# Kernel tuning notes

Hardware: AMD Instinct MI355X
Metric: run time of the kernel (lower is better)

The kernel has to match this reference:

```python
import jax, jax.numpy as jnp
import numpy as np
import math

def _ln(x, g, b, eps=1e-5):
    mu = x.mean(-1, keepdims=True)
    var = ((x - mu) ** 2).mean(-1, keepdims=True)
    return (x - mu) / jnp.sqrt(var + eps) * g + b

def _mha(x, in_w, in_b, out_w, out_b, nh):
    # torch nn.MultiheadAttention (batch_first, eval): q,k,v chunks of in_proj
    Bn, Nn, Dm = x.shape
    hd = Dm // nh
    q, k, v = jnp.split(x @ in_w.T + in_b, 3, axis=-1)
    sp = lambda t: t.reshape(Bn, Nn, nh, hd).transpose(0, 2, 1, 3)
    q, k, v = sp(q), sp(k), sp(v)
    a = jax.nn.softmax(jnp.einsum('bhid,bhjd->bhij', q, k) / math.sqrt(hd), axis=-1)
    y = jnp.einsum('bhij,bhjd->bhid', a, v).transpose(0, 2, 1, 3).reshape(Bn, Nn, Dm)
    return y @ out_w.T + out_b

def setup_inputs():
    key = jax.random.key(0)
    ks = iter(jax.random.split(key, 40))
    nrm = lambda shape: jax.random.normal(next(ks), shape, jnp.float32) * 0.02
    B, T, C, H, W = 2, 32, 3, 64, 64
    D, P, nL, nS = 512, 8, 6, 3
    N = (H // P) ** 2
    z = lambda *s: jnp.zeros(s, jnp.float32)
    o = lambda *s: jnp.ones(s, jnp.float32)
    return dict(
        x=jax.random.normal(next(ks), (B, T, C, H, W), jnp.float32),
        patch_w=nrm((D, C * P * P)), patch_b=z(D),
        tok_ln_g=o(D), tok_ln_b=z(D),
        spatial_pos=nrm((1, 1, N, D)), temporal_pos=nrm((1, T, 1, D)),
        snorm_g=o(D), snorm_b=z(D),
        sa_in_w=nrm((nS, 3 * D, D)), sa_in_b=z(nS, 3 * D),
        sa_out_w=nrm((nS, D, D)), sa_out_b=z(nS, D),
        ln1_g=o(nL, D), ln1_b=z(nL, D),
        kqv_w=nrm((nL, 3 * D, D)), kqv_b=z(nL, 3 * D),
        proj_w=nrm((nL, D, D)), proj_b=z(nL, D),
        ln2_g=o(nL, D), ln2_b=z(nL, D),
        fc_w=nrm((nL, 4 * D, D)), fc_b=z(nL, 4 * D),
        cproj_w=nrm((nL, D, 4 * D)), cproj_b=z(nL, D),
        lnf_g=o(D), lnf_b=z(D),
        th_w1=nrm((D // 2, D)), th_b1=z(D // 2), th_w2=nrm((1, D // 2)), th_b2=z(1),
        sh_w1=nrm((D // 2, D)), sh_b1=z(D // 2), sh_w2=nrm((1, D // 2)), sh_b2=z(1),
        pf_w1=nrm((D // 2, D)), pf_b1=z(D // 2), pf_w2=nrm((1, D // 2)), pf_b2=z(1),
    )

def reference(x, patch_w, patch_b, tok_ln_g, tok_ln_b, spatial_pos, temporal_pos,
              snorm_g, snorm_b, sa_in_w, sa_in_b, sa_out_w, sa_out_b,
              ln1_g, ln1_b, kqv_w, kqv_b, proj_w, proj_b, ln2_g, ln2_b,
              fc_w, fc_b, cproj_w, cproj_b, lnf_g, lnf_b,
              th_w1, th_b1, th_w2, th_b2, sh_w1, sh_b1, sh_w2, sh_b2,
              pf_w1, pf_b1, pf_w2, pf_b2):
    B, T, C, H, W = x.shape
    D = patch_w.shape[0]
    P = int(math.isqrt(patch_w.shape[1] // C))
    Hn, Wn = H // P, W // P
    N = Hn * Wn
    # Conv3d kernel=(1,P,P), stride=(1,P,P) == per-frame patchify + matmul
    patches = x.reshape(B, T, C, Hn, P, Wn, P).transpose(0, 1, 3, 5, 2, 4, 6).reshape(B, T, N, C * P * P)
    tok = _ln(patches @ patch_w.T + patch_b, tok_ln_g, tok_ln_b)
    tok = tok + spatial_pos + temporal_pos[:, :T]
    # per-frame spatial attention: identical math per frame -> batch over B*T
    s = tok.reshape(B * T, N, D)
    for i in range(sa_in_w.shape[0]):
        s = s + _mha(_ln(s, snorm_g, snorm_b), sa_in_w[i], sa_in_b[i], sa_out_w[i], sa_out_b[i], nh=4)
    L = T * N
    hid = s.reshape(B, L, D)
    nh = 8
    hd = D // nh
    mask = jnp.tril(jnp.ones((L, L), bool))  # causal over T*N tokens
    for i in range(kqv_w.shape[0]):
        a_in = _ln(hid, ln1_g[i], ln1_b[i])
        k, q, v = jnp.split(a_in @ kqv_w[i].T + kqv_b[i], 3, axis=-1)  # torch split order: k, q, v
        sp = lambda t: t.reshape(B, L, nh, hd).transpose(0, 2, 1, 3)
        q, k, v = sp(q), sp(k), sp(v)
        att = jnp.einsum('bhid,bhjd->bhij', q, k) / math.sqrt(hd)
        att = jax.nn.softmax(jnp.where(mask, att, -jnp.inf), axis=-1)
        y = jnp.einsum('bhij,bhjd->bhid', att, v).transpose(0, 2, 1, 3).reshape(B, L, D)
        hid = hid + y @ proj_w[i].T + proj_b[i]
        m_in = _ln(hid, ln2_g[i], ln2_b[i])
        h = jax.nn.gelu(m_in @ fc_w[i].T + fc_b[i], approximate=False)
        hid = hid + h @ cproj_w[i].T + cproj_b[i]
    hid = _ln(hid, lnf_g, lnf_b).reshape(B, T, N, D)
    head = lambda zz, w1, b1, w2, b2: jax.nn.leaky_relu(zz @ w1.T + b1, 0.2) @ w2.T + b2
    tf = hid.mean(axis=2)  # [B, T, D]
    temporal_score = head(tf[:, -1], th_w1, th_b1, th_w2, th_b2)  # [B, 1] (last timestep, full lengths)
    spatial_score = head(hid.mean(axis=1).mean(axis=1), sh_w1, sh_b1, sh_w2, sh_b2)
    per_frame_scores = head(tf, pf_w1, pf_b1, pf_w2, pf_b2)  # [B, T, 1]
    final_score = temporal_score + spatial_score + per_frame_scores.mean(axis=1)
    return (temporal_score, spatial_score, per_frame_scores, final_score)
```

## Files before the change

kernel.cpp:

```cpp
#include <hip/hip_runtime.h>
#include <hip/hip_bf16.h>
#include <math.h>

#define MTOK 4096

typedef __bf16 bf16x8 __attribute__((ext_vector_type(8)));
typedef float f32x4 __attribute__((ext_vector_type(4)));

__device__ __forceinline__ ushort f2bf(float f){
  __hip_bfloat16 h = __float2bfloat16(f);
  return *reinterpret_cast<ushort*>(&h);
}
__device__ __forceinline__ float bf2f(ushort u){
  return __uint_as_float(((uint)u) << 16);
}
__device__ __forceinline__ void gload_lds16(const void* g, void* l){
  __builtin_amdgcn_global_load_lds((__attribute__((address_space(1))) void*)(void*)g,
                                   (__attribute__((address_space(3))) void*)l, 16, 0, 0);
}

__device__ __forceinline__ float blockReduceSum(float v, float* red){
  #pragma unroll
  for (int off = 32; off; off >>= 1) v += __shfl_down(v, off, 64);
  int lane = threadIdx.x & 63, wid = threadIdx.x >> 6;
  __syncthreads();
  if (lane == 0) red[wid] = v;
  __syncthreads();
  float r = 0.f;
  int nw = blockDim.x >> 6;
  for (int i = 0; i < nw; i++) r += red[i];
  return r;
}
__device__ __forceinline__ float rowMax16(float v){
  #pragma unroll
  for (int m = 8; m; m >>= 1) v = fmaxf(v, __shfl_xor(v, m, 64));
  return v;
}
__device__ __forceinline__ float rowSum16(float v){
  #pragma unroll
  for (int m = 8; m; m >>= 1) v += __shfl_xor(v, m, 64);
  return v;
}

__global__ __launch_bounds__(256) void cvt_w_kernel(
    const float* __restrict__ src, ushort* __restrict__ dst, int n)
{
  int i = (blockIdx.x * 256 + threadIdx.x) * 8;
  float4 a = *(const float4*)(src + i);
  float4 b = *(const float4*)(src + i + 4);
  uint4 o;
  o.x = (uint)f2bf(a.x) | ((uint)f2bf(a.y) << 16);
  o.y = (uint)f2bf(a.z) | ((uint)f2bf(a.w) << 16);
  o.z = (uint)f2bf(b.x) | ((uint)f2bf(b.y) << 16);
  o.w = (uint)f2bf(b.z) | ((uint)f2bf(b.w) << 16);
  *(uint4*)(dst + i) = o;
}

#define OFF_PATCH 0u
#define OFF_SAIN  98304u
#define OFF_SAOUT 2457600u
#define OFF_KQV   3244032u
#define OFF_PROJ  7962624u
#define OFF_FC    9535488u
#define OFF_CPROJ 15826944u
#define W_TOTAL   22118400u
__global__ __launch_bounds__(256) void cvt_all_kernel(
    const float* __restrict__ pw, const float* __restrict__ sain,
    const float* __restrict__ saout, const float* __restrict__ kqv,
    const float* __restrict__ proj, const float* __restrict__ fc,
    const float* __restrict__ cproj, ushort* __restrict__ dst)
{
  int blk = blockIdx.x;
  const float* src; size_t off;
  if      (blk <    48){ src = pw;    off = OFF_PATCH; }
  else if (blk <  1200){ src = sain;  off = OFF_SAIN;  blk -= 48;   }
  else if (blk <  1584){ src = saout; off = OFF_SAOUT; blk -= 1200; }
  else if (blk <  3888){ src = kqv;   off = OFF_KQV;   blk -= 1584; }
  else if (blk <  4656){ src = proj;  off = OFF_PROJ;  blk -= 3888; }
  else if (blk <  7728){ src = fc;    off = OFF_FC;    blk -= 4656; }
  else                 { src = cproj; off = OFF_CPROJ; blk -= 7728; }
  size_t si = (size_t)blk*2048 + threadIdx.x*8;
  float4 a = *(const float4*)(src + si);
  float4 b = *(const float4*)(src + si + 4);
  uint4 o;
  o.x = (uint)f2bf(a.x) | ((uint)f2bf(a.y) << 16);
  o.y = (uint)f2bf(a.z) | ((uint)f2bf(a.w) << 16);
  o.z = (uint)f2bf(b.x) | ((uint)f2bf(b.y) << 16);
  o.w = (uint)f2bf(b.z) | ((uint)f2bf(b.w) << 16);
  *(uint4*)(dst + off + si) = o;
}

__global__ __launch_bounds__(256) void im2col_kernel(
    const float* __restrict__ x, ushort* __restrict__ Pm)
{
  int idx = blockIdx.x*256 + threadIdx.x;
  int m = idx / 24, e8 = idx % 24;
  int b = m >> 11, t = (m >> 6) & 31, n = m & 63;
  int hn = n >> 3, wn = n & 7;
  int c = e8 >> 3, ph = e8 & 7;
  const float* src = x + (((size_t)(b*32 + t)*3 + c)*64 + hn*8 + ph)*64 + wn*8;
  float4 a = *(const float4*)src;
  float4 bq = *(const float4*)(src + 4);
  uint4 o;
  o.x = (uint)f2bf(a.x) | ((uint)f2bf(a.y) << 16);
  o.y = (uint)f2bf(a.z) | ((uint)f2bf(a.w) << 16);
  o.z = (uint)f2bf(bq.x) | ((uint)f2bf(bq.y) << 16);
  o.w = (uint)f2bf(bq.z) | ((uint)f2bf(bq.w) << 16);
  *(uint4*)(Pm + (size_t)m*192 + e8*8) = o;
}

__global__ __launch_bounds__(256) void ln_pos_kernel(
    const float* __restrict__ in, float* __restrict__ out,
    const float* __restrict__ g, const float* __restrict__ b,
    const float* __restrict__ spos, const float* __restrict__ tpos)
{
  int r = blockIdx.x*4 + (threadIdx.x >> 6);
  int lane = threadIdx.x & 63;
  int n = r & 63, t = (r >> 6) & 31;
  const float* row = in + (size_t)r*512 + lane*8;
  float4 v0 = *(const float4*)row;
  float4 v1 = *(const float4*)(row + 4);
  float s = v0.x+v0.y+v0.z+v0.w+v1.x+v1.y+v1.z+v1.w;
  float q = v0.x*v0.x+v0.y*v0.y+v0.z*v0.z+v0.w*v0.w+v1.x*v1.x+v1.y*v1.y+v1.z*v1.z+v1.w*v1.w;
  #pragma unroll
  for (int m = 1; m < 64; m <<= 1){ s += __shfl_xor(s, m, 64); q += __shfl_xor(q, m, 64); }
  float mu = s*(1.f/512.f);
  float inv = rsqrtf(q*(1.f/512.f) - mu*mu + 1e-5f);
  const float* gp = g + lane*8;
  const float* bp = b + lane*8;
  const float* sp = spos + n*512 + lane*8;
  const float* tp = tpos + t*512 + lane*8;
  float* op = out + (size_t)r*512 + lane*8;
  #pragma unroll
  for (int e = 0; e < 2; e++){
    float4 vv = e ? v1 : v0;
    float4 gg = *(const float4*)(gp + e*4);
    float4 bb = *(const float4*)(bp + e*4);
    float4 ss = *(const float4*)(sp + e*4);
    float4 tt = *(const float4*)(tp + e*4);
    float4 oo;
    oo.x = (vv.x-mu)*inv*gg.x + bb.x + ss.x + tt.x;
    oo.y = (vv.y-mu)*inv*gg.y + bb.y + ss.y + tt.y;
    oo.z = (vv.z-mu)*inv*gg.z + bb.z + ss.z + tt.z;
    oo.w = (vv.w-mu)*inv*gg.w + bb.w + ss.w + tt.w;
    *(float4*)(op + e*4) = oo;
  }
}

__global__ __launch_bounds__(256) void ln_bf16_kernel(
    const float* __restrict__ in, ushort* __restrict__ out,
    const float* __restrict__ g, const float* __restrict__ b)
{
  int r = blockIdx.x*4 + (threadIdx.x >> 6);
  int lane = threadIdx.x & 63;
  const float* row = in + (size_t)r*512 + lane*8;
  float4 v0 = *(const float4*)row;
  float4 v1 = *(const float4*)(row + 4);
  float s = v0.x+v0.y+v0.z+v0.w+v1.x+v1.y+v1.z+v1.w;
  float q = v0.x*v0.x+v0.y*v0.y+v0.z*v0.z+v0.w*v0.w+v1.x*v1.x+v1.y*v1.y+v1.z*v1.z+v1.w*v1.w;
  #pragma unroll
  for (int m = 1; m < 64; m <<= 1){ s += __shfl_xor(s, m, 64); q += __shfl_xor(q, m, 64); }
  float mu = s*(1.f/512.f);
  float inv = rsqrtf(q*(1.f/512.f) - mu*mu + 1e-5f);
  float4 g0 = *(const float4*)(g + lane*8);
  float4 g1 = *(const float4*)(g + lane*8 + 4);
  float4 b0 = *(const float4*)(b + lane*8);
  float4 b1 = *(const float4*)(b + lane*8 + 4);
  uint4 o;
  o.x = (uint)f2bf((v0.x-mu)*inv*g0.x + b0.x) | ((uint)f2bf((v0.y-mu)*inv*g0.y + b0.y) << 16);
  o.y = (uint)f2bf((v0.z-mu)*inv*g0.z + b0.z) | ((uint)f2bf((v0.w-mu)*inv*g0.w + b0.w) << 16);
  o.z = (uint)f2bf((v1.x-mu)*inv*g1.x + b1.x) | ((uint)f2bf((v1.y-mu)*inv*g1.y + b1.y) << 16);
  o.w = (uint)f2bf((v1.z-mu)*inv*g1.z + b1.z) | ((uint)f2bf((v1.w-mu)*inv*g1.w + b1.w) << 16);
  *(uint4*)(out + (size_t)r*512 + lane*8) = o;
}

template<int BM, int BN, bool GELU, bool BF16OUT>
__global__ __launch_bounds__(256) void gemm2_kernel(
    const ushort* __restrict__ X, const ushort* __restrict__ Wb,
    const float* __restrict__ bias, const float* __restrict__ res,
    void* __restrict__ Yv, int M, int Nn, int K)
{
  constexpr int WROWS = (BN == 128) ? 2 : 4;
  constexpr int WM = BM / WROWS;
  constexpr int FM = WM / 16;
  constexpr int FN = 4;
  __shared__ __attribute__((aligned(16))) char smem[2*(BM+BN)*128];
  char* Xs0 = smem;
  char* Ws0 = smem + BM*128;
  char* Xs1 = smem + (BM+BN)*128;
  char* Ws1 = Xs1 + BM*128;
  int tid = threadIdx.x, lane = tid & 63, wv = tid >> 6;
  int bm = blockIdx.y * BM, bn = blockIdx.x * BN;
  int wm, wn;
  if (BN == 128){ wm = (wv >> 1) * WM; wn = (wv & 1) * 64; }
  else          { wm = wv * WM;        wn = 0; }

  f32x4 acc[FM][FN];
  #pragma unroll
  for (int i = 0; i < FM; i++)
    #pragma unroll
    for (int j = 0; j < FN; j++){ f32x4 z = {0.f,0.f,0.f,0.f}; acc[i][j] = z; }

  int rowoff = wv*8 + (lane >> 3);
  int colsrc = ((lane & 7) ^ (lane >> 3)) * 16;

  auto stage = [&](char* Xd, char* Wd, int k0){
    #pragma unroll
    for (int i = 0; i < BM/32; i++){
      int row = i*32 + rowoff;
      gload_lds16((const char*)(X + (size_t)(bm + row)*K + k0) + colsrc,
                  Xd + (i*32 + wv*8)*128);
    }
    #pragma unroll
    for (int i = 0; i < BN/32; i++){
      int row = i*32 + rowoff;
      gload_lds16((const char*)(Wb + (size_t)(bn + row)*K + k0) + colsrc,
                  Wd + (i*32 + wv*8)*128);
    }
  };

  stage(Xs0, Ws0, 0);
  __syncthreads();
  int nt = K >> 6;
  for (int t = 0; t < nt; t++){
    char* Xc = (t & 1) ? Xs1 : Xs0;
    char* Wc = (t & 1) ? Ws1 : Ws0;
    if (t + 1 < nt) stage((t & 1) ? Xs0 : Xs1, (t & 1) ? Ws0 : Ws1, (t+1)*64);
    #pragma unroll
    for (int kc = 0; kc < 2; kc++){
      bf16x8 a[FM], b[FN];
      #pragma unroll
      for (int f = 0; f < FM; f++){
        int ra = wm + f*16 + (lane & 15);
        a[f] = *(const bf16x8*)(Xc + ra*128 + ((kc*64 + (lane>>4)*16) ^ ((ra & 7) << 4)));
      }
      #pragma unroll
      for (int f = 0; f < FN; f++){
        int rb = wn + f*16 + (lane & 15);
        b[f] = *(const bf16x8*)(Wc + rb*128 + ((kc*64 + (lane>>4)*16) ^ ((rb & 7) << 4)));
      }
      #pragma unroll
      for (int i = 0; i < FM; i++)
        #pragma unroll
        for (int j = 0; j < FN; j++)
          acc[i][j] = __builtin_amdgcn_mfma_f32_16x16x32_bf16(a[i], b[j], acc[i][j], 0, 0, 0);
    }
    __syncthreads();
  }
  int col0 = lane & 15;
  float bv[FN];
  #pragma unroll
  for (int fn = 0; fn < FN; fn++) bv[fn] = bias[bn + wn + fn*16 + col0];
  #pragma unroll
  for (int fm = 0; fm < FM; fm++){
    #pragma unroll
    for (int r = 0; r < 4; r++){
      int m = bm + wm + fm*16 + (lane >> 4)*4 + r;
      #pragma unroll
      for (int fn = 0; fn < FN; fn++){
        int n = bn + wn + fn*16 + col0;
        float v = acc[fm][fn][r] + bv[fn];
        if (res) v += res[(size_t)m*Nn + n];
        if (GELU) v = 0.5f * v * (1.f + erff(v * 0.70710678118654752440f));
        if (BF16OUT) ((ushort*)Yv)[(size_t)m*Nn + n] = f2bf(v);
        else         ((float*) Yv)[(size_t)m*Nn + n] = v;
      }
    }
  }
}

__global__ __launch_bounds__(256) void spatial_attn_mfma_kernel(
    const ushort* __restrict__ qkv, ushort* __restrict__ y)
{
  __shared__ __attribute__((aligned(16))) char Ks[64*256];
  __shared__ __attribute__((aligned(16))) char Vt[128*128];
  __shared__ __attribute__((aligned(16))) char Ps[64*128];
  int bt = blockIdx.x, h = blockIdx.y;
  int tid = threadIdx.x, lane = tid & 63, w = tid >> 6;
  const ushort* base = qkv + (size_t)bt*64*1536 + (size_t)h*128;
  const float scale = 0.08838834764831845f;

  int qrow = w*16 + (lane & 15);
  bf16x8 qa[4];
  #pragma unroll
  for (int kc = 0; kc < 4; kc++)
    qa[kc] = *(const bf16x8*)(base + (size_t)qrow*1536 + kc*32 + (lane>>4)*8);

  #pragma unroll
  for (int i = 0; i < 4; i++){
    int row = w*16 + i*4 + (lane >> 4);
    const char* src = (const char*)(base + (size_t)row*1536 + 512) + (((lane & 15) ^ (row & 15)) * 16);
    char* dst = Ks + (w*16 + i*4)*256;
    gload_lds16(src, dst);
  }
  {
    int vj = (tid & 31) * 2;
    int d0 = (tid >> 5) * 16;
    const ushort* v0p = base + (size_t)vj*1536 + 1024 + d0;
    const ushort* v1p = v0p + 1536;
    uint4 a0 = *(const uint4*)(v0p);
    uint4 a1 = *(const uint4*)(v0p + 8);
    uint4 b0 = *(const uint4*)(v1p);
    uint4 b1 = *(const uint4*)(v1p + 8);
    uint av[8] = {a0.x, a0.y, a0.z, a0.w, a1.x, a1.y, a1.z, a1.w};
    uint bv[8] = {b0.x, b0.y, b0.z, b0.w, b1.x, b1.y, b1.z, b1.w};
    int cb = 4 * (tid & 31);
    #pragma unroll
    for (int e = 0; e < 8; e++){
      int dl = d0 + e*2, dh = dl + 1;
      uint vlo = (av[e] & 0xffffu) | ((bv[e] & 0xffffu) << 16);
      uint vhi = (av[e] >> 16) | (bv[e] & 0xffff0000u);
      *(uint*)(Vt + dl*128 + (cb ^ ((dl & 7) << 4))) = vlo;
      *(uint*)(Vt + dh*128 + (cb ^ ((dh & 7) << 4))) = vhi;
    }
  }
  __syncthreads();

  f32x4 zero4 = {0.f,0.f,0.f,0.f};
  f32x4 accS[4];
  __builtin_amdgcn_s_setprio(1);
  #pragma unroll
  for (int jt = 0; jt < 4; jt++){
    accS[jt] = zero4;
    #pragma unroll
    for (int kc = 0; kc < 4; kc++){
      int krow = jt*16 + (lane & 15);
      bf16x8 kb = *(const bf16x8*)(Ks + krow*256 + ((kc*64 + (lane>>4)*16) ^ ((krow & 15) << 4)));
      accS[jt] = __builtin_amdgcn_mfma_f32_16x16x32_bf16(qa[kc], kb, accS[jt], 0, 0, 0);
    }
  }
  __builtin_amdgcn_s_setprio(0);
  float l_sum[4];
  #pragma unroll
  for (int r = 0; r < 4; r++){
    float mx = fmaxf(fmaxf(accS[0][r], accS[1][r]), fmaxf(accS[2][r], accS[3][r]));
    mx = rowMax16(mx);
    int prow = w*16 + (lane>>4)*4 + r;
    int swz = (prow & 7) << 4;
    char* pbase = Ps + prow*128;
    float ps = 0.f;
    #pragma unroll
    for (int jt = 0; jt < 4; jt++){
      float p = __expf((accS[jt][r] - mx) * scale);
      ushort pb = f2bf(p);
      *(ushort*)(pbase + ((2*(jt*16 + (lane & 15))) ^ swz)) = pb;
      ps += bf2f(pb);
    }
    l_sum[r] = rowSum16(ps);
  }
  bf16x8 pa[2];
  #pragma unroll
  for (int kc2 = 0; kc2 < 2; kc2++){
    int prow = w*16 + (lane & 15);
    pa[kc2] = *(const bf16x8*)(Ps + prow*128 + ((kc2*64 + (lane>>4)*16) ^ ((prow & 7) << 4)));
  }
  f32x4 o[8];
  __builtin_amdgcn_s_setprio(1);
  #pragma unroll
  for (int dt = 0; dt < 8; dt++){
    o[dt] = zero4;
    #pragma unroll
    for (int kc2 = 0; kc2 < 2; kc2++){
      int vrow = dt*16 + (lane & 15);
      bf16x8 vb = *(const bf16x8*)(Vt + vrow*128 + ((kc2*64 + (lane>>4)*16) ^ ((vrow & 7) << 4)));
      o[dt] = __builtin_amdgcn_mfma_f32_16x16x32_bf16(pa[kc2], vb, o[dt], 0, 0, 0);
    }
  }
  __builtin_amdgcn_s_setprio(0);
  #pragma unroll
  for (int r = 0; r < 4; r++){
    float invl = 1.f / l_sum[r];
    int token = bt*64 + w*16 + (lane>>4)*4 + r;
    ushort* yrow = y + (size_t)token*512 + h*128;
    #pragma unroll
    for (int dt = 0; dt < 8; dt++)
      yrow[dt*16 + (lane & 15)] = f2bf(o[dt][r] * invl);
  }
}

__global__ __launch_bounds__(256) void temporal_attn_split_kernel(
    const ushort* __restrict__ qkv, ushort* __restrict__ Op, float* __restrict__ ml)
{
  __shared__ __attribute__((aligned(16))) char Ks[64*128];
  __shared__ __attribute__((aligned(16))) char Vt[64*128];
  __shared__ __attribute__((aligned(16))) char Ps[64*128];
  int id = blockIdx.x;
  int bh = id & 15;
  int rest = id >> 4;
  int qt = 31 - (rest >> 1);
  int half = rest & 1;
  int b = bh >> 3, h = bh & 7;
  int tid = threadIdx.x, lane = tid & 63, w = tid >> 6;
  const ushort* base = qkv + (size_t)(b*2048)*1536 + h*64;

  int nk = qt + 1;
  int ktm = (nk + 1) >> 1;
  int kt0 = half ? ktm : 0;
  int kt1 = half ? nk : ktm;

  int qrow = qt*64 + w*16 + (lane & 15);
  bf16x8 qa[2];
  #pragma unroll
  for (int kc = 0; kc < 2; kc++)
    qa[kc] = *(const bf16x8*)(base + (size_t)qrow*1536 + 512 + kc*32 + (lane>>4)*8);

  f32x4 zero4 = {0.f,0.f,0.f,0.f};
  f32x4 o[4];
  float m_old[4], l_sum[4];
  #pragma unroll
  for (int dt = 0; dt < 4; dt++) o[dt] = zero4;
  #pragma unroll
  for (int r = 0; r < 4; r++){ m_old[r] = -1e30f; l_sum[r] = 0.f; }

  int kcolsrc = ((lane & 7) ^ (lane >> 3)) * 16;
  int vj = tid & 63;
  int vd0 = (tid >> 6) * 16;

  for (int kt = kt0; kt < kt1; kt++){
    __syncthreads();
    #pragma unroll
    for (int i = 0; i < 2; i++){
      int row = w*16 + i*8 + (lane >> 3);
      gload_lds16((const char*)(base + (size_t)(kt*64 + row)*1536) + kcolsrc,
                  Ks + (w*16 + i*8)*128);
    }
    {
      const ushort* vrow = base + (size_t)(kt*64 + vj)*1536 + 1024 + vd0;
      uint4 p0 = *(const uint4*)(vrow);
      uint4 p1 = *(const uint4*)(vrow + 8);
      uint vals[8] = {p0.x, p0.y, p0.z, p0.w, p1.x, p1.y, p1.z, p1.w};
      #pragma unroll
      for (int e = 0; e < 8; e++){
        int d0 = vd0 + e*2;
        *(ushort*)(Vt + d0*128     + ((2*vj) ^ (( d0    & 7) << 4))) = (ushort)(vals[e] & 0xffff);
        *(ushort*)(Vt + (d0+1)*128 + ((2*vj) ^ (((d0+1) & 7) << 4))) = (ushort)(vals[e] >> 16);
      }
    }
    __syncthreads();

    f32x4 accS[4];
    __builtin_amdgcn_s_setprio(1);
    #pragma unroll
    for (int jt = 0; jt < 4; jt++){
      accS[jt] = zero4;
      #pragma unroll
      for (int kc = 0; kc < 2; kc++){
        int krow = jt*16 + (lane & 15);
        bf16x8 kb = *(const bf16x8*)(Ks + krow*128 + ((kc*64 + (lane>>4)*16) ^ ((krow & 7) << 4)));
        accS[jt] = __builtin_amdgcn_mfma_f32_16x16x32_bf16(qa[kc], kb, accS[jt], 0, 0, 0);
      }
    }
    __builtin_amdgcn_s_setprio(0);
    if (kt == qt){
      #pragma unroll
      for (int jt = 0; jt < 4; jt++){
        int gj = kt*64 + jt*16 + (lane & 15);
        #pragma unroll
        for (int r = 0; r < 4; r++){
          int gi = qt*64 + w*16 + (lane>>4)*4 + r;
          if (gj > gi) accS[jt][r] = -1e30f;
        }
      }
    }
    #pragma unroll
    for (int r = 0; r < 4; r++){
      float mloc = fmaxf(fmaxf(accS[0][r], accS[1][r]), fmaxf(accS[2][r], accS[3][r])) * 0.125f;
      mloc = rowMax16(mloc);
      float mnew = fmaxf(m_old[r], mloc);
      float corr = __expf(m_old[r] - mnew);
      int prow = w*16 + (lane>>4)*4 + r;
      int swz = (prow & 7) << 4;
      char* pbase = Ps + prow*128;
      float ps = 0.f;
      #pragma unroll
      for (int jt = 0; jt < 4; jt++){
        float p = __expf(accS[jt][r]*0.125f - mnew);
        ushort pb = f2bf(p);
        *(ushort*)(pbase + ((2*(jt*16 + (lane & 15))) ^ swz)) = pb;
        ps += bf2f(pb);
      }
      ps = rowSum16(ps);
      l_sum[r] = l_sum[r]*corr + ps;
      m_old[r] = mnew;
      #pragma unroll
      for (int dt = 0; dt < 4; dt++) o[dt][r] *= corr;
    }
    bf16x8 pa[2];
    #pragma unroll
    for (int kc2 = 0; kc2 < 2; kc2++){
      int prow = w*16 + (lane & 15);
      pa[kc2] = *(const bf16x8*)(Ps + prow*128 + ((kc2*64 + (lane>>4)*16) ^ ((prow & 7) << 4)));
    }
    __builtin_amdgcn_s_setprio(1);
    #pragma unroll
    for (int dt = 0; dt < 4; dt++){
      #pragma unroll
      for (int kc2 = 0; kc2 < 2; kc2++){
        int vrow = dt*16 + (lane & 15);
        bf16x8 vb = *(const bf16x8*)(Vt + vrow*128 + ((kc2*64 + (lane>>4)*16) ^ ((vrow & 7) << 4)));
        o[dt] = __builtin_amdgcn_mfma_f32_16x16x32_bf16(pa[kc2], vb, o[dt], 0, 0, 0);
      }
    }
    __builtin_amdgcn_s_setprio(0);
  }
  size_t tokbase = (size_t)half*4096 + (size_t)b*2048;
  #pragma unroll
  for (int r = 0; r < 4; r++){
    int token = qt*64 + w*16 + (lane>>4)*4 + r;
    ushort* yrow = Op + (tokbase + token)*512 + h*64;
    #pragma unroll
    for (int dt = 0; dt < 4; dt++)
      yrow[dt*16 + (lane & 15)] = f2bf(o[dt][r]);
    if ((lane & 15) == 0){
      float* mlp = ml + ((tokbase + token)*8 + h)*2;
      mlp[0] = m_old[r];
      mlp[1] = l_sum[r];
    }
  }
}

__global__ __launch_bounds__(256) void attn_merge_kernel(
    const ushort* __restrict__ Op, const float* __restrict__ ml, ushort* __restrict__ Ef)
{
  int tok = blockIdx.x*4 + (threadIdx.x >> 6);
  int l6 = threadIdx.x & 63;
  int h = l6 >> 3, d0 = (l6 & 7)*8;
  int e = h*64 + d0;
  const float* m1p = ml + ((size_t)tok*8 + h)*2;
  const float* m2p = ml + (((size_t)4096 + tok)*8 + h)*2;
  float m1 = m1p[0], l1 = m1p[1];
  float m2 = m2p[0], l2 = m2p[1];
  float mm = fmaxf(m1, m2);
  float w1 = __expf(m1 - mm), w2 = __expf(m2 - mm);
  float inv = 1.f / (w1*l1 + w2*l2);
  uint4 a = *(const uint4*)(Op + (size_t)tok*512 + e);
  uint4 bq = *(const uint4*)(Op + ((size_t)4096 + tok)*512 + e);
  uint av[4] = {a.x, a.y, a.z, a.w};
  uint bv[4] = {bq.x, bq.y, bq.z, bq.w};
  uint4 o;
  uint ov[4];
  #pragma unroll
  for (int p = 0; p < 4; p++){
    float x0 = (w1*bf2f((ushort)(av[p] & 0xffff)) + w2*bf2f((ushort)(bv[p] & 0xffff))) * inv;
    float x1 = (w1*bf2f((ushort)(av[p] >> 16))    + w2*bf2f((ushort)(bv[p] >> 16)))    * inv;
    ov[p] = (uint)f2bf(x0) | ((uint)f2bf(x1) << 16);
  }
  o.x = ov[0]; o.y = ov[1]; o.z = ov[2]; o.w = ov[3];
  *(uint4*)(Ef + (size_t)tok*512 + e) = o;
}

__global__ __launch_bounds__(256) void reduce_tf_kernel(const ushort* __restrict__ hid, float* __restrict__ tf){
  int bt = blockIdx.x, tid = threadIdx.x;
  for (int d = tid; d < 512; d += 256){
    float s = 0.f;
    for (int n = 0; n < 64; n++) s += bf2f(hid[((size_t)bt*64 + n)*512 + d]);
    tf[(size_t)bt*512 + d] = s * (1.f/64.f);
  }
}

__global__ __launch_bounds__(256) void head_kernel(
    const float* __restrict__ tf,
    const float* __restrict__ th_w1, const float* __restrict__ th_b1,
    const float* __restrict__ th_w2, const float* __restrict__ th_b2,
    const float* __restrict__ sh_w1, const float* __restrict__ sh_b1,
    const float* __restrict__ sh_w2, const float* __restrict__ sh_b2,
    const float* __restrict__ pf_w1, const float* __restrict__ pf_b1,
    const float* __restrict__ pf_w2, const float* __restrict__ pf_b2,
    float* __restrict__ out)
{
  __shared__ float z[512];
  __shared__ float red[4];
  int bi = blockIdx.x, tid = threadIdx.x;
  const float *w1, *b1, *w2, *b2;
  float* dst;
  if (bi < 64){
    w1 = pf_w1; b1 = pf_b1; w2 = pf_w2; b2 = pf_b2; dst = out + 4 + bi;
    z[tid]       = tf[(size_t)bi*512 + tid];
    z[tid + 256] = tf[(size_t)bi*512 + tid + 256];
  } else if (bi < 66){
    int b = bi - 64;
    w1 = th_w1; b1 = th_b1; w2 = th_w2; b2 = th_b2; dst = out + b;
    z[tid]       = tf[(size_t)(b*32 + 31)*512 + tid];
    z[tid + 256] = tf[(size_t)(b*32 + 31)*512 + tid + 256];
  } else {
    int b = bi - 66;
    w1 = sh_w1; b1 = sh_b1; w2 = sh_w2; b2 = sh_b2; dst = out + 2 + b;
    float s0 = 0.f, s1 = 0.f;
    for (int t = 0; t < 32; t++){
      s0 += tf[(size_t)(b*32 + t)*512 + tid];
      s1 += tf[(size_t)(b*32 + t)*512 + tid + 256];
    }
    z[tid] = s0 * (1.f/32.f); z[tid + 256] = s1 * (1.f/32.f);
  }
  __syncthreads();
  float a = b1[tid];
  const float* wrow = w1 + (size_t)tid * 512;
  for (int k = 0; k < 512; k++) a = fmaf(wrow[k], z[k], a);
  a = (a > 0.f) ? a : 0.2f * a;
  float s = blockReduceSum(a * w2[tid], red);
  if (tid == 0) *dst = s + b2[0];
}

__global__ __launch_bounds__(64) void final_kernel(float* __restrict__ out){
  int b = threadIdx.x;
  if (b < 2){
    float s = 0.f;
    for (int t = 0; t < 32; t++) s += out[4 + b*32 + t];
    out[68 + b] = out[b] + out[2 + b] + s * (1.f/32.f);
  }
}

extern "C" void kernel_launch(void* const* d_in, const int* in_sizes, int n_in,
                              void* d_out, int out_size, void* d_ws, size_t ws_size,
                              hipStream_t stream)
{
  const float* x          = (const float*)d_in[0];
  const float* patch_w    = (const float*)d_in[1];
  const float* patch_b    = (const float*)d_in[2];
  const float* tok_ln_g   = (const float*)d_in[3];
  const float* tok_ln_b   = (const float*)d_in[4];
  const float* spatial_pos= (const float*)d_in[5];
  const float* temporal_pos=(const float*)d_in[6];
  const float* snorm_g    = (const float*)d_in[7];
  const float* snorm_b    = (const float*)d_in[8];
  const float* sa_in_w    = (const float*)d_in[9];
  const float* sa_in_b    = (const float*)d_in[10];
  const float* sa_out_w   = (const float*)d_in[11];
  const float* sa_out_b   = (const float*)d_in[12];
  const float* ln1_g      = (const float*)d_in[13];
  const float* ln1_b      = (const float*)d_in[14];
  const float* kqv_w      = (const float*)d_in[15];
  const float* kqv_b      = (const float*)d_in[16];
  const float* proj_w     = (const float*)d_in[17];
  const float* proj_b     = (const float*)d_in[18];
  const float* ln2_g      = (const float*)d_in[19];
  const float* ln2_b      = (const float*)d_in[20];
  const float* fc_w       = (const float*)d_in[21];
  const float* fc_b       = (const float*)d_in[22];
  const float* cproj_w    = (const float*)d_in[23];
  const float* cproj_b    = (const float*)d_in[24];
  const float* lnf_g      = (const float*)d_in[25];
  const float* lnf_b      = (const float*)d_in[26];
  const float* th_w1 = (const float*)d_in[27];
  const float* th_b1 = (const float*)d_in[28];
  const float* th_w2 = (const float*)d_in[29];
  const float* th_b2 = (const float*)d_in[30];
  const float* sh_w1 = (const float*)d_in[31];
  const float* sh_b1 = (const float*)d_in[32];
  const float* sh_w2 = (const float*)d_in[33];
  const float* sh_b2 = (const float*)d_in[34];
  const float* pf_w1 = (const float*)d_in[35];
  const float* pf_b1 = (const float*)d_in[36];
  const float* pf_w2 = (const float*)d_in[37];
  const float* pf_b2 = (const float*)d_in[38];

  float* out = (float*)d_out;
  char* p = (char*)d_ws;
  float*  A  = (float*)p;      p += (size_t)MTOK*512*4;
  ushort* Ru = (ushort*)p;     p += (size_t)MTOK*2048*2;
  ushort* Bf = (ushort*)p;     p += (size_t)MTOK*512*2;
  ushort* Ef = (ushort*)p;     p += (size_t)MTOK*512*2;
  float*  tfp = (float*)p;     p += (size_t)64*512*4;
  ushort* OpB = (ushort*)p;    p += (size_t)2*MTOK*512*2;
  float*  mlB = (float*)p;     p += (size_t)2*MTOK*8*2*4;
  ushort* Wslot = (ushort*)p;  p += (size_t)1048576*2;
  ushort* Wall = (ushort*)p;   p += (size_t)W_TOTAL*2;
  float*  Pf = (float*)Ru;
  ushort* Pm = Ef;

  const size_t NEED_BIG = (size_t)((char*)p - (char*)d_ws);
  const bool big = (ws_size >= NEED_BIG);

  if (big){
    cvt_all_kernel<<<10800, 256, 0, stream>>>(patch_w, sa_in_w, sa_out_w, kqv_w,
                                              proj_w, fc_w, cproj_w, Wall);
  }
  auto W = [&](const float* src, size_t arena_off, size_t nelem) -> const ushort* {
    if (big) return Wall + arena_off;
    cvt_w_kernel<<<(int)(nelem/2048), 256, 0, stream>>>(src, Wslot, (int)nelem);
    return Wslot;
  };

  im2col_kernel<<<384, 256, 0, stream>>>(x, Pm);
  gemm2_kernel<64,64,false,false><<<dim3(8, 64), 256, 0, stream>>>(
      Pm, W(patch_w, OFF_PATCH, 512*192), patch_b, nullptr, Pf, MTOK, 512, 192);
  ln_pos_kernel<<<1024, 256, 0, stream>>>(Pf, A, tok_ln_g, tok_ln_b, spatial_pos, temporal_pos);

  for (int i = 0; i < 3; i++){
    ln_bf16_kernel<<<1024, 256, 0, stream>>>(A, Bf, snorm_g, snorm_b);
    gemm2_kernel<64,128,false,true><<<dim3(12, 64), 256, 0, stream>>>(
        Bf, W(sa_in_w + (size_t)i*1536*512, OFF_SAIN + (size_t)i*786432, 1536*512),
        sa_in_b + (size_t)i*1536, nullptr, Ru, MTOK, 1536, 512);
    spatial_attn_mfma_kernel<<<dim3(64, 4), 256, 0, stream>>>(Ru, Ef);
    gemm2_kernel<64,64,false,false><<<dim3(8, 64), 256, 0, stream>>>(
        Ef, W(sa_out_w + (size_t)i*512*512, OFF_SAOUT + (size_t)i*262144, 512*512),
        sa_out_b + (size_t)i*512, A, A, MTOK, 512, 512);
  }
  for (int i = 0; i < 6; i++){
    ln_bf16_kernel<<<1024, 256, 0, stream>>>(A, Bf, ln1_g + (size_t)i*512, ln1_b + (size_t)i*512);
    gemm2_kernel<64,128,false,true><<<dim3(12, 64), 256, 0, stream>>>(
        Bf, W(kqv_w + (size_t)i*1536*512, OFF_KQV + (size_t)i*786432, 1536*512),
        kqv_b + (size_t)i*1536, nullptr, Ru, MTOK, 1536, 512);
    temporal_attn_split_kernel<<<1024, 256, 0, stream>>>(Ru, OpB, mlB);
    attn_merge_kernel<<<1024, 256, 0, stream>>>(OpB, mlB, Ef);
    gemm2_kernel<64,64,false,false><<<dim3(8, 64), 256, 0, stream>>>(
        Ef, W(proj_w + (size_t)i*512*512, OFF_PROJ + (size_t)i*262144, 512*512),
        proj_b + (size_t)i*512, A, A, MTOK, 512, 512);
    ln_bf16_kernel<<<1024, 256, 0, stream>>>(A, Bf, ln2_g + (size_t)i*512, ln2_b + (size_t)i*512);
    gemm2_kernel<128,128,true,true><<<dim3(16, 32), 256, 0, stream>>>(
        Bf, W(fc_w + (size_t)i*2048*512, OFF_FC + (size_t)i*1048576, 2048*512),
        fc_b + (size_t)i*2048, nullptr, Ru, MTOK, 2048, 512);
    gemm2_kernel<64,64,false,false><<<dim3(8, 64), 256, 0, stream>>>(
        Ru, W(cproj_w + (size_t)i*512*2048, OFF_CPROJ + (size_t)i*1048576, 512*2048),
        cproj_b + (size_t)i*512, A, A, MTOK, 512, 2048);
  }
  ln_bf16_kernel<<<1024, 256, 0, stream>>>(A, Bf, lnf_g, lnf_b);
  reduce_tf_kernel<<<64, 256, 0, stream>>>(Bf, tfp);
  head_kernel<<<68, 256, 0, stream>>>(tfp, th_w1, th_b1, th_w2, th_b2,
                                      sh_w1, sh_b1, sh_w2, sh_b2,
                                      pf_w1, pf_b1, pf_w2, pf_b2, out);
  final_kernel<<<1, 64, 0, stream>>>(out);
}
```

Baseline: 860.9 us.

## Split temporal attention KV range four ways and shrink FC GEMM tile

Generalizes the split-KV causal temporal attention from two chunks to a template parameter S. When the workspace is large enough it launches four chunks (2048 blocks) with extra partial-output and max/sum buffers, and the merge kernel combines S partials. This is meant to spread the long causal rows over more blocks and improve load balance. Separately, the FC GEMM tile is reduced from 128x128 to 64x128, doubling its grid for better occupancy, at the cost of more partial-output traffic and less reuse per tile.

```diff
diff --git a/kernel.cpp b/kernel.cpp
--- a/kernel.cpp
+++ b/kernel.cpp
@@ -378,8 +378,11 @@
   }
 }
 
+template<int S>
 __global__ __launch_bounds__(256) void temporal_attn_split_kernel(
-    const ushort* __restrict__ qkv, ushort* __restrict__ Op, float* __restrict__ ml)
+    const ushort* __restrict__ qkv,
+    ushort* __restrict__ Opa, ushort* __restrict__ Opb,
+    float* __restrict__ mla, float* __restrict__ mlb)
 {
   __shared__ __attribute__((aligned(16))) char Ks[64*128];
   __shared__ __attribute__((aligned(16))) char Vt[64*128];
@@ -387,16 +390,18 @@
   int id = blockIdx.x;
   int bh = id & 15;
   int rest = id >> 4;
-  int qt = 31 - (rest >> 1);
-  int half = rest & 1;
+  int qt = 31 - (rest / S);
+  int chunk = rest % S;
   int b = bh >> 3, h = bh & 7;
   int tid = threadIdx.x, lane = tid & 63, w = tid >> 6;
   const ushort* base = qkv + (size_t)(b*2048)*1536 + h*64;
 
   int nk = qt + 1;
-  int ktm = (nk + 1) >> 1;
-  int kt0 = half ? ktm : 0;
-  int kt1 = half ? nk : ktm;
+  int kt0 = (nk * chunk) / S;
+  int kt1 = (nk * (chunk + 1)) / S;
+
+  ushort* Oc = (chunk < 2) ? (Opa + (size_t)chunk*MTOK*512) : (Opb + (size_t)(chunk-2)*MTOK*512);
+  float*  mc = (chunk < 2) ? (mla + (size_t)chunk*MTOK*16)  : (mlb + (size_t)(chunk-2)*MTOK*16);
 
   int qrow = qt*64 + w*16 + (lane & 15);
   bf16x8 qa[2];
@@ -503,49 +508,62 @@
     }
     __builtin_amdgcn_s_setprio(0);
   }
-  size_t tokbase = (size_t)half*4096 + (size_t)b*2048;
   #pragma unroll
   for (int r = 0; r < 4; r++){
     int token = qt*64 + w*16 + (lane>>4)*4 + r;
-    ushort* yrow = Op + (tokbase + token)*512 + h*64;
+    ushort* yrow = Oc + ((size_t)b*2048 + token)*512 + h*64;
     #pragma unroll
     for (int dt = 0; dt < 4; dt++)
       yrow[dt*16 + (lane & 15)] = f2bf(o[dt][r]);
     if ((lane & 15) == 0){
-      float* mlp = ml + ((tokbase + token)*8 + h)*2;
+      float* mlp = mc + (((size_t)b*2048 + token)*8 + h)*2;
       mlp[0] = m_old[r];
       mlp[1] = l_sum[r];
     }
   }
 }
 
+template<int S>
 __global__ __launch_bounds__(256) void attn_merge_kernel(
-    const ushort* __restrict__ Op, const float* __restrict__ ml, ushort* __restrict__ Ef)
+    const ushort* __restrict__ Opa, const ushort* __restrict__ Opb,
+    const float* __restrict__ mla, const float* __restrict__ mlb,
+    ushort* __restrict__ Ef)
 {
   int tok = blockIdx.x*4 + (threadIdx.x >> 6);
   int l6 = threadIdx.x & 63;
   int h = l6 >> 3, d0 = (l6 & 7)*8;
   int e = h*64 + d0;
-  const float* m1p = ml + ((size_t)tok*8 + h)*2;
-  const float* m2p = ml + (((size_t)4096 + tok)*8 + h)*2;
-  float m1 = m1p[0], l1 = m1p[1];
-  float m2 = m2p[0], l2 = m2p[1];
-  float mm = fmaxf(m1, m2);
-  float w1 = __expf(m1 - mm), w2 = __expf(m2 - mm);
-  float inv = 1.f / (w1*l1 + w2*l2);
-  uint4 a = *(const uint4*)(Op + (size_t)tok*512 + e);
-  uint4 bq = *(const uint4*)(Op + ((size_t)4096 + tok)*512 + e);
-  uint av[4] = {a.x, a.y, a.z, a.w};
-  uint bv[4] = {bq.x, bq.y, bq.z, bq.w};
-  uint4 o;
+  float mv[S], lv[S];
+  float mm = -1e30f;
+  #pragma unroll
+  for (int c = 0; c < S; c++){
+    const float* mp = ((c < 2) ? (mla + (size_t)c*MTOK*16) : (mlb + (size_t)(c-2)*MTOK*16))
+                      + ((size_t)tok*8 + h)*2;
+    mv[c] = mp[0]; lv[c] = mp[1];
+    mm = fmaxf(mm, mv[c]);
+  }
+  float acc[8] = {};
+  float lsum = 0.f;
+  #pragma unroll
+  for (int c = 0; c < S; c++){
+    float wc = __expf(mv[c] - mm);
+    lsum += wc * lv[c];
+    const ushort* op = ((c < 2) ? (Opa + (size_t)c*MTOK*512) : (Opb + (size_t)(c-2)*MTOK*512))
+                       + (size_t)tok*512 + e;
+    uint4 a = *(const uint4*)op;
+    uint av[4] = {a.x, a.y, a.z, a.w};
+    #pragma unroll
+    for (int p = 0; p < 4; p++){
+      acc[2*p]   += wc * bf2f((ushort)(av[p] & 0xffff));
+      acc[2*p+1] += wc * bf2f((ushort)(av[p] >> 16));
+    }
+  }
+  float inv = 1.f / lsum;
   uint ov[4];
   #pragma unroll
-  for (int p = 0; p < 4; p++){
-    float x0 = (w1*bf2f((ushort)(av[p] & 0xffff)) + w2*bf2f((ushort)(bv[p] & 0xffff))) * inv;
-    float x1 = (w1*bf2f((ushort)(av[p] >> 16))    + w2*bf2f((ushort)(bv[p] >> 16)))    * inv;
-    ov[p] = (uint)f2bf(x0) | ((uint)f2bf(x1) << 16);
-  }
-  o.x = ov[0]; o.y = ov[1]; o.z = ov[2]; o.w = ov[3];
+  for (int p = 0; p < 4; p++)
+    ov[p] = (uint)f2bf(acc[2*p]*inv) | ((uint)f2bf(acc[2*p+1]*inv) << 16);
+  uint4 o; o.x = ov[0]; o.y = ov[1]; o.z = ov[2]; o.w = ov[3];
   *(uint4*)(Ef + (size_t)tok*512 + e) = o;
 }
 
@@ -665,11 +683,15 @@
   float*  mlB = (float*)p;     p += (size_t)2*MTOK*8*2*4;
   ushort* Wslot = (ushort*)p;  p += (size_t)1048576*2;
   ushort* Wall = (ushort*)p;   p += (size_t)W_TOTAL*2;
+  const size_t NEED_BIG = (size_t)(p - (char*)d_ws);
+  ushort* OpT = (ushort*)p;    p += (size_t)2*MTOK*512*2;
+  float*  mlT = (float*)p;     p += (size_t)2*MTOK*8*2*4;
+  const size_t NEED_4WAY = (size_t)(p - (char*)d_ws);
   float*  Pf = (float*)Ru;
   ushort* Pm = Ef;
 
-  const size_t NEED_BIG = (size_t)((char*)p - (char*)d_ws);
-  const bool big = (ws_size >= NEED_BIG);
+  const bool big  = (ws_size >= NEED_BIG);
+  const bool big4 = (ws_size >= NEED_4WAY);
 
   if (big){
     cvt_all_kernel<<<10800, 256, 0, stream>>>(patch_w, sa_in_w, sa_out_w, kqv_w,
@@ -701,13 +723,18 @@
     gemm2_kernel<64,128,false,true><<<dim3(12, 64), 256, 0, stream>>>(
         Bf, W(kqv_w + (size_t)i*1536*512, OFF_KQV + (size_t)i*786432, 1536*512),
         kqv_b + (size_t)i*1536, nullptr, Ru, MTOK, 1536, 512);
-    temporal_attn_split_kernel<<<1024, 256, 0, stream>>>(Ru, OpB, mlB);
-    attn_merge_kernel<<<1024, 256, 0, stream>>>(OpB, mlB, Ef);
+    if (big4){
+      temporal_attn_split_kernel<4><<<2048, 256, 0, stream>>>(Ru, OpB, OpT, mlB, mlT);
+      attn_merge_kernel<4><<<1024, 256, 0, stream>>>(OpB, OpT, mlB, mlT, Ef);
+    } else {
+      temporal_attn_split_kernel<2><<<1024, 256, 0, stream>>>(Ru, OpB, OpB, mlB, mlB);
+      attn_merge_kernel<2><<<1024, 256, 0, stream>>>(OpB, OpB, mlB, mlB, Ef);
+    }
     gemm2_kernel<64,64,false,false><<<dim3(8, 64), 256, 0, stream>>>(
         Ef, W(proj_w + (size_t)i*512*512, OFF_PROJ + (size_t)i*262144, 512*512),
         proj_b + (size_t)i*512, A, A, MTOK, 512, 512);
     ln_bf16_kernel<<<1024, 256, 0, stream>>>(A, Bf, ln2_g + (size_t)i*512, ln2_b + (size_t)i*512);
-    gemm2_kernel<128,128,true,true><<<dim3(16, 32), 256, 0, stream>>>(
+    gemm2_kernel<64,128,true,true><<<dim3(16, 64), 256, 0, stream>>>(
         Bf, W(fc_w + (size_t)i*2048*512, OFF_FC + (size_t)i*1048576, 2048*512),
         fc_b + (size_t)i*2048, nullptr, Ru, MTOK, 2048, 512);
     gemm2_kernel<64,64,false,false><<<dim3(8, 64), 256, 0, stream>>>(
```

Measured after the change: 858.7 us. No clear change (-0.2%).
